# Performance work log

Measured on AMD Instinct MI355X. Metric: run time of the kernel, lower is better.

Reference implementation:

```python
import jax, jax.numpy as jnp
import numpy as np

B, S, K, N, G = 4, 16, 8192, 8192, 128
NUM_GROUPS = K // G

def setup_inputs() -> dict:
    key = jax.random.key(0)
    k1, k2, k3, k4, k5 = jax.random.split(key, 5)
    x = jax.random.normal(k1, (B, S, K), dtype=jnp.float32)
    qweight = jax.random.randint(k2, (K, N), -128, 128, dtype=jnp.int32)
    # small positive scales like real quantizers produce
    scales = jax.random.uniform(k3, (NUM_GROUPS, N), dtype=jnp.float32) * 0.01 + 1e-4
    zeros = jax.random.uniform(k4, (NUM_GROUPS, N), dtype=jnp.float32) * 2.0 - 1.0
    bias = jax.random.normal(k5, (N,), dtype=jnp.float32)
    return {"x": x, "qweight": qweight, "scales": scales, "zeros": zeros,
            "bias": bias, "group_size": G}

def reference(x, qweight, scales, zeros, bias, group_size):
    # Expand per-group scale/zero along K: [num_groups, N] -> [K, N]
    Kdim = qweight.shape[0]
    if scales.shape[0] == 1:
        scale_exp = jnp.broadcast_to(scales, (Kdim, scales.shape[1]))
        zero_exp = jnp.broadcast_to(zeros, (Kdim, zeros.shape[1]))
    else:
        scale_exp = jnp.repeat(scales, group_size, axis=0)[:Kdim]
        zero_exp = jnp.repeat(zeros, group_size, axis=0)[:Kdim]
    # Dequantize: W[k, n] = (q - zero) * scale
    weight_fp = (qweight.astype(x.dtype) - zero_exp) * scale_exp  # [K, N]
    out = jnp.einsum('bsk,kn->bsn', x, weight_fp) + bias
    return out
```

## Files before the change

### kernel.cpp

```cpp
#include <hip/hip_runtime.h>

typedef __attribute__((ext_vector_type(8))) short short8;
typedef __attribute__((ext_vector_type(8))) unsigned short ushort8;
typedef __attribute__((ext_vector_type(4))) unsigned short ushort4v;
typedef __attribute__((ext_vector_type(4))) int int4v;
typedef __attribute__((ext_vector_type(4))) float f32x4;

#define Mdim 64
#define Kdim 8192
#define Ndim 8192
#define GRP 128
#define NGRP 64
#define KSPLIT 4
#define NG2 (NGRP / KSPLIT)
#define BN 128

#define SWZ(row, kk) ((row)*128 + ((kk) ^ (8*((((row) >> 3) ^ (row)) & 7))))

__device__ __forceinline__ unsigned short f2bf(float f) {
    unsigned int u = __builtin_bit_cast(unsigned int, f);
    u += 0x7FFFu + ((u >> 16) & 1u);
    return (unsigned short)(u >> 16);
}
__device__ __forceinline__ float bf2f(unsigned short h) {
    unsigned int u = ((unsigned int)h) << 16;
    return __builtin_bit_cast(float, u);
}

__global__ void prep_kernel(const float* __restrict__ x,
                            unsigned short* __restrict__ xh,
                            unsigned short* __restrict__ xl,
                            float* __restrict__ xsum) {
    const int tid = threadIdx.x;
    const int u = blockIdx.x * 8 + (tid >> 5);
    const int g = u & (NGRP - 1);
    const int m = u >> 6;
    const int lane = tid & 31;
    const int k = g * GRP + lane * 4;
    f32x4 v = *(const f32x4*)(x + (size_t)m * Kdim + k);
    ushort4v hv, lv;
    float s = 0.f;
#pragma unroll
    for (int i = 0; i < 4; ++i) {
        unsigned short h = f2bf(v[i]);
        hv[i] = h;
        lv[i] = f2bf(v[i] - bf2f(h));
        s += v[i];
    }
    *(ushort4v*)(xh + (size_t)m * Kdim + k) = hv;
    *(ushort4v*)(xl + (size_t)m * Kdim + k) = lv;
#pragma unroll
    for (int off = 16; off > 0; off >>= 1) s += __shfl_down(s, off, 32);
    if (lane == 0) xsum[g * Mdim + m] = s;
}

__launch_bounds__(512, 2)
__global__ void qlin_kernel(const unsigned short* __restrict__ xh,
                            const unsigned short* __restrict__ xl,
                            const int* __restrict__ qw,
                            const float* __restrict__ scales,
                            const float* __restrict__ zeros,
                            const float* __restrict__ xsum,
                            float* __restrict__ pout) {
    __shared__ unsigned short lq[2][128 * 128];
    __shared__ unsigned short lxh[2][64 * 128];
    __shared__ unsigned short lxl[2][64 * 128];
    __shared__ float ls[NG2][128];
    __shared__ float lz[NG2][128];
    __shared__ float lxs[NG2][64];

    const int tid = threadIdx.x;
    const int kh = blockIdx.x & (KSPLIT - 1);
    const int n0 = (blockIdx.x >> 2) * BN;
    const int g0 = kh * NG2;

    const int w = tid >> 6;
    const int l = tid & 63;
    const int lcol = l & 15;
    const int lhi = l >> 4;
    const int mt = (w >> 2) * 32;
    const int ns = (w & 3) * 32;

    const int qc = tid & 31;
    const int qr = tid >> 5;
    const int xc = tid & 15;
    const int xm = tid >> 4;

    const int c0 = n0 + ns + lcol;
    const int c1 = c0 + 16;

    int4v qv[8];
    ushort8 xga, xgb, xgc, xgd;

    auto LOADX = [&](int g) {
        const size_t kb = (size_t)g * GRP + xc * 8;
        xga = *(const ushort8*)(xh + (size_t)xm * Kdim + kb);
        xgb = *(const ushort8*)(xh + (size_t)(xm + 32) * Kdim + kb);
        xgc = *(const ushort8*)(xl + (size_t)xm * Kdim + kb);
        xgd = *(const ushort8*)(xl + (size_t)(xm + 32) * Kdim + kb);
    };
    auto LOADQ = [&](int g) {
        const size_t kb = (size_t)g * GRP + qr * 8;
        const int nc = n0 + qc * 4;
#pragma unroll
        for (int j = 0; j < 8; ++j)
            qv[j] = *(const int4v*)(qw + (kb + j) * Ndim + nc);
    };
    auto WRITEX = [&](int b) {
        *(ushort8*)&lxh[b][SWZ(xm, xc * 8)] = xga;
        *(ushort8*)&lxh[b][SWZ(xm + 32, xc * 8)] = xgb;
        *(ushort8*)&lxl[b][SWZ(xm, xc * 8)] = xgc;
        *(ushort8*)&lxl[b][SWZ(xm + 32, xc * 8)] = xgd;
    };
    auto WRITEQ = [&](int b) {
#pragma unroll
        for (int i = 0; i < 4; ++i) {
            int4v pk;
#pragma unroll
            for (int t = 0; t < 4; ++t) {
                unsigned lo = __builtin_bit_cast(unsigned, (float)qv[2 * t][i]) >> 16;
                unsigned hi = __builtin_bit_cast(unsigned, (float)qv[2 * t + 1][i]) & 0xFFFF0000u;
                pk[t] = (int)(lo | hi);
            }
            *(int4v*)&lq[b][SWZ(qc * 4 + i, qr * 8)] = pk;
        }
    };

    f32x4 acc00 = {0,0,0,0}, acc01 = {0,0,0,0}, acc10 = {0,0,0,0}, acc11 = {0,0,0,0};

    {
        const int tg = tid >> 5, tc = tid & 31;
        f32x4 sv = *(const f32x4*)(scales + (size_t)(g0 + tg) * Ndim + n0 + tc * 4);
        f32x4 zv = *(const f32x4*)(zeros + (size_t)(g0 + tg) * Ndim + n0 + tc * 4);
        float x0 = xsum[(g0 + (tid >> 6)) * Mdim + (tid & 63)];
        float x1 = xsum[(g0 + ((tid + 512) >> 6)) * Mdim + (tid & 63)];
        LOADX(g0);
        LOADQ(g0);
        *(f32x4*)&ls[tg][tc * 4] = sv;
        *(f32x4*)&lz[tg][tc * 4] = zv;
        (&lxs[0][0])[tid] = x0;
        (&lxs[0][0])[tid + 512] = x1;
        WRITEX(0);
        WRITEQ(0);
        if (1 < NG2) { LOADX(g0 + 1); LOADQ(g0 + 1); }
        asm volatile("s_waitcnt lgkmcnt(0)" ::: "memory");
        __builtin_amdgcn_s_barrier();
    }

    for (int g = 0; g < NG2; ++g) {
        const int b = g & 1;

        f32x4 p00 = {0,0,0,0}, p01 = {0,0,0,0}, p10 = {0,0,0,0}, p11 = {0,0,0,0};
#pragma unroll
        for (int ks = 0; ks < 4; ++ks) {
            const int kk = ks * 32 + lhi * 8;
            short8 bq0 = *(const short8*)&lq[b][SWZ(ns + lcol, kk)];
            short8 bq1 = *(const short8*)&lq[b][SWZ(ns + 16 + lcol, kk)];
            short8 ah0 = *(const short8*)&lxh[b][SWZ(mt + lcol, kk)];
            short8 al0 = *(const short8*)&lxl[b][SWZ(mt + lcol, kk)];
            short8 ah1 = *(const short8*)&lxh[b][SWZ(mt + 16 + lcol, kk)];
            short8 al1 = *(const short8*)&lxl[b][SWZ(mt + 16 + lcol, kk)];
            p00 = __builtin_amdgcn_mfma_f32_16x16x32_bf16(ah0, bq0, p00, 0, 0, 0);
            p00 = __builtin_amdgcn_mfma_f32_16x16x32_bf16(al0, bq0, p00, 0, 0, 0);
            p01 = __builtin_amdgcn_mfma_f32_16x16x32_bf16(ah0, bq1, p01, 0, 0, 0);
            p01 = __builtin_amdgcn_mfma_f32_16x16x32_bf16(al0, bq1, p01, 0, 0, 0);
            p10 = __builtin_amdgcn_mfma_f32_16x16x32_bf16(ah1, bq0, p10, 0, 0, 0);
            p10 = __builtin_amdgcn_mfma_f32_16x16x32_bf16(al1, bq0, p10, 0, 0, 0);
            p11 = __builtin_amdgcn_mfma_f32_16x16x32_bf16(ah1, bq1, p11, 0, 0, 0);
            p11 = __builtin_amdgcn_mfma_f32_16x16x32_bf16(al1, bq1, p11, 0, 0, 0);
        }
        {
            const float s0 = ls[g][ns + lcol],      z0 = lz[g][ns + lcol];
            const float s1 = ls[g][ns + 16 + lcol], z1 = lz[g][ns + 16 + lcol];
            f32x4 xs0 = *(const f32x4*)&lxs[g][mt + lhi * 4];
            f32x4 xs1 = *(const f32x4*)&lxs[g][mt + 16 + lhi * 4];
#pragma unroll
            for (int r = 0; r < 4; ++r) {
                acc00[r] += s0 * (p00[r] - z0 * xs0[r]);
                acc01[r] += s1 * (p01[r] - z1 * xs0[r]);
                acc10[r] += s0 * (p10[r] - z0 * xs1[r]);
                acc11[r] += s1 * (p11[r] - z1 * xs1[r]);
            }
        }

        if (g + 1 < NG2) {
            WRITEX(b ^ 1);
            if (g + 2 < NG2) {
                LOADX(g0 + g + 2);
                __builtin_amdgcn_sched_barrier(0);
            }
            WRITEQ(b ^ 1);
            if (g + 2 < NG2) {
                LOADQ(g0 + g + 2);
                __builtin_amdgcn_sched_barrier(0);
            }
            asm volatile("s_waitcnt lgkmcnt(0)" ::: "memory");
            __builtin_amdgcn_s_barrier();
        }
    }

    const size_t ob = (size_t)kh * Mdim * Ndim;
#pragma unroll
    for (int r = 0; r < 4; ++r) {
        pout[ob + (size_t)(mt + lhi * 4 + r) * Ndim + c0] = acc00[r];
        pout[ob + (size_t)(mt + lhi * 4 + r) * Ndim + c1] = acc01[r];
        pout[ob + (size_t)(mt + 16 + lhi * 4 + r) * Ndim + c0] = acc10[r];
        pout[ob + (size_t)(mt + 16 + lhi * 4 + r) * Ndim + c1] = acc11[r];
    }
}

__global__ void reduce_kernel(const float* __restrict__ pout,
                              const float* __restrict__ bias,
                              float* __restrict__ out) {
    const size_t e = ((size_t)blockIdx.x * 256 + threadIdx.x) * 4;
    const int n = (int)(e & (Ndim - 1));
    f32x4 a = *(const f32x4*)(bias + n);
#pragma unroll
    for (int s = 0; s < KSPLIT; ++s) {
        f32x4 ppart = *(const f32x4*)(pout + (size_t)s * Mdim * Ndim + e);
#pragma unroll
        for (int r = 0; r < 4; ++r) a[r] += ppart[r];
    }
    *(f32x4*)(out + e) = a;
}

extern "C" void kernel_launch(void* const* d_in, const int* in_sizes, int n_in,
                              void* d_out, int out_size, void* d_ws, size_t ws_size,
                              hipStream_t stream) {
    const float* x = (const float*)d_in[0];
    const int* qw = (const int*)d_in[1];
    const float* scales = (const float*)d_in[2];
    const float* zeros = (const float*)d_in[3];
    const float* bias = (const float*)d_in[4];

    unsigned short* xh = (unsigned short*)d_ws;
    unsigned short* xl = xh + (size_t)Mdim * Kdim;
    float* xsum = (float*)(xl + (size_t)Mdim * Kdim);
    float* pout = xsum + NGRP * Mdim;
    float* out = (float*)d_out;

    prep_kernel<<<512, 256, 0, stream>>>(x, xh, xl, xsum);
    qlin_kernel<<<(Ndim / BN) * KSPLIT, 512, 0, stream>>>(xh, xl, qw, scales, zeros, xsum, pout);
    reduce_kernel<<<(Mdim * Ndim / 4) / 256, 256, 0, stream>>>(pout, bias, out);
}
```

Measured before the change: 56.23 us.

## Deepen weight prefetch to three stages and replace split-K reduction with atomics

Quantized weight tiles are now prefetched two groups ahead using two alternating register sets, so global load latency has more time to hide behind MFMA work. The split-K partial-sum buffer and the separate reduce kernel are removed. Instead, an init kernel writes the bias into the output and each K-split block atomically adds its tile. This cuts the partial-sum write and re-read traffic, but it adds atomic contention, more register pressure from the extra weight buffer, and a non-deterministic summation order.

```diff
diff --git a/kernel.cpp b/kernel.cpp
--- a/kernel.cpp
+++ b/kernel.cpp
@@ -54,6 +54,35 @@
     if (lane == 0) xsum[g * Mdim + m] = s;
 }
 
+__global__ void init_kernel(const float* __restrict__ bias,
+                            float* __restrict__ out) {
+    const size_t e = ((size_t)blockIdx.x * 256 + threadIdx.x) * 4;
+    const int n = (int)(e & (Ndim - 1));
+    *(f32x4*)(out + e) = *(const f32x4*)(bias + n);
+}
+
+#define LOADQ_M(dst, g) do {                                                  \
+    const size_t kb_ = (size_t)(g) * GRP + qr * 8;                            \
+    const int nc_ = n0 + qc * 4;                                              \
+    _Pragma("unroll")                                                         \
+    for (int j = 0; j < 8; ++j)                                               \
+        dst[j] = *(const int4v*)(qw + (kb_ + j) * Ndim + nc_);                \
+} while (0)
+
+#define WRITEQ_M(src, b) do {                                                 \
+    _Pragma("unroll")                                                         \
+    for (int i = 0; i < 4; ++i) {                                             \
+        int4v pk_;                                                            \
+        _Pragma("unroll")                                                     \
+        for (int t = 0; t < 4; ++t) {                                         \
+            unsigned lo_ = __builtin_bit_cast(unsigned, (float)src[2*t][i]) >> 16;           \
+            unsigned hi_ = __builtin_bit_cast(unsigned, (float)src[2*t+1][i]) & 0xFFFF0000u; \
+            pk_[t] = (int)(lo_ | hi_);                                        \
+        }                                                                     \
+        *(int4v*)&lq[b][SWZ(qc * 4 + i, qr * 8)] = pk_;                       \
+    }                                                                         \
+} while (0)
+
 __launch_bounds__(512, 2)
 __global__ void qlin_kernel(const unsigned short* __restrict__ xh,
                             const unsigned short* __restrict__ xl,
@@ -61,7 +90,7 @@
                             const float* __restrict__ scales,
                             const float* __restrict__ zeros,
                             const float* __restrict__ xsum,
-                            float* __restrict__ pout) {
+                            float* __restrict__ out) {
     __shared__ unsigned short lq[2][128 * 128];
     __shared__ unsigned short lxh[2][64 * 128];
     __shared__ unsigned short lxl[2][64 * 128];
@@ -89,7 +118,7 @@
     const int c0 = n0 + ns + lcol;
     const int c1 = c0 + 16;
 
-    int4v qv[8];
+    int4v qva[8], qvb[8];
     ushort8 xga, xgb, xgc, xgd;
 
     auto LOADX = [&](int g) {
@@ -99,57 +128,17 @@
         xgc = *(const ushort8*)(xl + (size_t)xm * Kdim + kb);
         xgd = *(const ushort8*)(xl + (size_t)(xm + 32) * Kdim + kb);
     };
-    auto LOADQ = [&](int g) {
-        const size_t kb = (size_t)g * GRP + qr * 8;
-        const int nc = n0 + qc * 4;
-#pragma unroll
-        for (int j = 0; j < 8; ++j)
-            qv[j] = *(const int4v*)(qw + (kb + j) * Ndim + nc);
-    };
     auto WRITEX = [&](int b) {
         *(ushort8*)&lxh[b][SWZ(xm, xc * 8)] = xga;
         *(ushort8*)&lxh[b][SWZ(xm + 32, xc * 8)] = xgb;
         *(ushort8*)&lxl[b][SWZ(xm, xc * 8)] = xgc;
         *(ushort8*)&lxl[b][SWZ(xm + 32, xc * 8)] = xgd;
     };
-    auto WRITEQ = [&](int b) {
-#pragma unroll
-        for (int i = 0; i < 4; ++i) {
-            int4v pk;
-#pragma unroll
-            for (int t = 0; t < 4; ++t) {
-                unsigned lo = __builtin_bit_cast(unsigned, (float)qv[2 * t][i]) >> 16;
-                unsigned hi = __builtin_bit_cast(unsigned, (float)qv[2 * t + 1][i]) & 0xFFFF0000u;
-                pk[t] = (int)(lo | hi);
-            }
-            *(int4v*)&lq[b][SWZ(qc * 4 + i, qr * 8)] = pk;
-        }
-    };
 
     f32x4 acc00 = {0,0,0,0}, acc01 = {0,0,0,0}, acc10 = {0,0,0,0}, acc11 = {0,0,0,0};
 
-    {
-        const int tg = tid >> 5, tc = tid & 31;
-        f32x4 sv = *(const f32x4*)(scales + (size_t)(g0 + tg) * Ndim + n0 + tc * 4);
-        f32x4 zv = *(const f32x4*)(zeros + (size_t)(g0 + tg) * Ndim + n0 + tc * 4);
-        float x0 = xsum[(g0 + (tid >> 6)) * Mdim + (tid & 63)];
-        float x1 = xsum[(g0 + ((tid + 512) >> 6)) * Mdim + (tid & 63)];
-        LOADX(g0);
-        LOADQ(g0);
-        *(f32x4*)&ls[tg][tc * 4] = sv;
-        *(f32x4*)&lz[tg][tc * 4] = zv;
-        (&lxs[0][0])[tid] = x0;
-        (&lxs[0][0])[tid + 512] = x1;
-        WRITEX(0);
-        WRITEQ(0);
-        if (1 < NG2) { LOADX(g0 + 1); LOADQ(g0 + 1); }
-        asm volatile("s_waitcnt lgkmcnt(0)" ::: "memory");
-        __builtin_amdgcn_s_barrier();
-    }
-
-    for (int g = 0; g < NG2; ++g) {
+    auto COMPUTE = [&](int g) {
         const int b = g & 1;
-
         f32x4 p00 = {0,0,0,0}, p01 = {0,0,0,0}, p10 = {0,0,0,0}, p11 = {0,0,0,0};
 #pragma unroll
         for (int ks = 0; ks < 4; ++ks) {
@@ -169,59 +158,72 @@
             p11 = __builtin_amdgcn_mfma_f32_16x16x32_bf16(ah1, bq1, p11, 0, 0, 0);
             p11 = __builtin_amdgcn_mfma_f32_16x16x32_bf16(al1, bq1, p11, 0, 0, 0);
         }
-        {
-            const float s0 = ls[g][ns + lcol],      z0 = lz[g][ns + lcol];
-            const float s1 = ls[g][ns + 16 + lcol], z1 = lz[g][ns + 16 + lcol];
-            f32x4 xs0 = *(const f32x4*)&lxs[g][mt + lhi * 4];
-            f32x4 xs1 = *(const f32x4*)&lxs[g][mt + 16 + lhi * 4];
-#pragma unroll
-            for (int r = 0; r < 4; ++r) {
-                acc00[r] += s0 * (p00[r] - z0 * xs0[r]);
-                acc01[r] += s1 * (p01[r] - z1 * xs0[r]);
-                acc10[r] += s0 * (p10[r] - z0 * xs1[r]);
-                acc11[r] += s1 * (p11[r] - z1 * xs1[r]);
-            }
+        const float s0 = ls[g][ns + lcol],      z0 = lz[g][ns + lcol];
+        const float s1 = ls[g][ns + 16 + lcol], z1 = lz[g][ns + 16 + lcol];
+        f32x4 xs0 = *(const f32x4*)&lxs[g][mt + lhi * 4];
+        f32x4 xs1 = *(const f32x4*)&lxs[g][mt + 16 + lhi * 4];
+#pragma unroll
+        for (int r = 0; r < 4; ++r) {
+            acc00[r] += s0 * (p00[r] - z0 * xs0[r]);
+            acc01[r] += s1 * (p01[r] - z1 * xs0[r]);
+            acc10[r] += s0 * (p10[r] - z0 * xs1[r]);
+            acc11[r] += s1 * (p11[r] - z1 * xs1[r]);
         }
-
-        if (g + 1 < NG2) {
-            WRITEX(b ^ 1);
-            if (g + 2 < NG2) {
-                LOADX(g0 + g + 2);
-                __builtin_amdgcn_sched_barrier(0);
-            }
-            WRITEQ(b ^ 1);
-            if (g + 2 < NG2) {
-                LOADQ(g0 + g + 2);
-                __builtin_amdgcn_sched_barrier(0);
-            }
-            asm volatile("s_waitcnt lgkmcnt(0)" ::: "memory");
-            __builtin_amdgcn_s_barrier();
-        }
-    }
-
-    const size_t ob = (size_t)kh * Mdim * Ndim;
+    };
+
+    {
+        const int tg = tid >> 5, tc = tid & 31;
+        f32x4 sv = *(const f32x4*)(scales + (size_t)(g0 + tg) * Ndim + n0 + tc * 4);
+        f32x4 zv = *(const f32x4*)(zeros + (size_t)(g0 + tg) * Ndim + n0 + tc * 4);
+        float x0 = xsum[(g0 + (tid >> 6)) * Mdim + (tid & 63)];
+        float x1 = xsum[(g0 + ((tid + 512) >> 6)) * Mdim + (tid & 63)];
+        LOADX(g0);
+        LOADQ_M(qva, g0);
+        *(f32x4*)&ls[tg][tc * 4] = sv;
+        *(f32x4*)&lz[tg][tc * 4] = zv;
+        (&lxs[0][0])[tid] = x0;
+        (&lxs[0][0])[tid + 512] = x1;
+        WRITEX(0);
+        WRITEQ_M(qva, 0);
+        LOADX(g0 + 1);
+        LOADQ_M(qvb, g0 + 1);
+        LOADQ_M(qva, g0 + 2);
+        asm volatile("s_waitcnt lgkmcnt(0)" ::: "memory");
+        __builtin_amdgcn_s_barrier();
+    }
+
+#define STEP(G, DSET) do {                                                    \
+    const int g_ = (G);                                                       \
+    COMPUTE(g_);                                                              \
+    if (g_ + 1 < NG2) {                                                       \
+        WRITEX((g_ & 1) ^ 1);                      \
+        if (g_ + 2 < NG2) {                                                   \
+            LOADX(g0 + g_ + 2);                                               \
+            __builtin_amdgcn_sched_barrier(0);                                \
+        }                                                                     \
+        WRITEQ_M(DSET, (g_ & 1) ^ 1);              \
+        if (g_ + 3 < NG2) {                                                   \
+            LOADQ_M(DSET, g0 + g_ + 3);             \
+            __builtin_amdgcn_sched_barrier(0);                                \
+        }                                                                     \
+        asm volatile("s_waitcnt lgkmcnt(0)" ::: "memory");                    \
+        __builtin_amdgcn_s_barrier();                                         \
+    }                                                                         \
+} while (0)
+
+    for (int gg = 0; gg < NG2; gg += 2) {
+        STEP(gg, qvb);
+        STEP(gg + 1, qva);
+    }
+#undef STEP
+
 #pragma unroll
     for (int r = 0; r < 4; ++r) {
-        pout[ob + (size_t)(mt + lhi * 4 + r) * Ndim + c0] = acc00[r];
-        pout[ob + (size_t)(mt + lhi * 4 + r) * Ndim + c1] = acc01[r];
-        pout[ob + (size_t)(mt + 16 + lhi * 4 + r) * Ndim + c0] = acc10[r];
-        pout[ob + (size_t)(mt + 16 + lhi * 4 + r) * Ndim + c1] = acc11[r];
-    }
-}
-
-__global__ void reduce_kernel(const float* __restrict__ pout,
-                              const float* __restrict__ bias,
-                              float* __restrict__ out) {
-    const size_t e = ((size_t)blockIdx.x * 256 + threadIdx.x) * 4;
-    const int n = (int)(e & (Ndim - 1));
-    f32x4 a = *(const f32x4*)(bias + n);
-#pragma unroll
-    for (int s = 0; s < KSPLIT; ++s) {
-        f32x4 ppart = *(const f32x4*)(pout + (size_t)s * Mdim * Ndim + e);
-#pragma unroll
-        for (int r = 0; r < 4; ++r) a[r] += ppart[r];
-    }
-    *(f32x4*)(out + e) = a;
+        atomicAdd(out + (size_t)(mt + lhi * 4 + r) * Ndim + c0, acc00[r]);
+        atomicAdd(out + (size_t)(mt + lhi * 4 + r) * Ndim + c1, acc01[r]);
+        atomicAdd(out + (size_t)(mt + 16 + lhi * 4 + r) * Ndim + c0, acc10[r]);
+        atomicAdd(out + (size_t)(mt + 16 + lhi * 4 + r) * Ndim + c1, acc11[r]);
+    }
 }
 
 extern "C" void kernel_launch(void* const* d_in, const int* in_sizes, int n_in,
@@ -236,10 +238,9 @@
     unsigned short* xh = (unsigned short*)d_ws;
     unsigned short* xl = xh + (size_t)Mdim * Kdim;
     float* xsum = (float*)(xl + (size_t)Mdim * Kdim);
-    float* pout = xsum + NGRP * Mdim;
     float* out = (float*)d_out;
 
     prep_kernel<<<512, 256, 0, stream>>>(x, xh, xl, xsum);
-    qlin_kernel<<<(Ndim / BN) * KSPLIT, 512, 0, stream>>>(xh, xl, qw, scales, zeros, xsum, pout);
-    reduce_kernel<<<(Mdim * Ndim / 4) / 256, 256, 0, stream>>>(pout, bias, out);
-}
+    init_kernel<<<(Mdim * Ndim / 4) / 256, 256, 0, stream>>>(bias, out);
+    qlin_kernel<<<(Ndim / BN) * KSPLIT, 512, 0, stream>>>(xh, xl, qw, scales, zeros, xsum, out);
+}
```

After: 58.27 us. +3.6%, slower.

## Fuse split-K reduction into GEMM kernel via last-block atomic counter

Applied to the files above, without the earlier changes.

Removes the separate reduce kernel launch. Each N-tile keeps an atomic counter, reset in the prep kernel, and the last split-K block to finish sums the partial outputs plus bias for its tile. This saves one kernel launch and lets the reduction overlap with other blocks still computing. The cost is a threadfence, an atomic per block, and serial reduce work in the final block of each tile.

```diff
diff --git a/kernel.cpp b/kernel.cpp
--- a/kernel.cpp
+++ b/kernel.cpp
@@ -30,8 +30,10 @@
 __global__ void prep_kernel(const float* __restrict__ x,
                             unsigned short* __restrict__ xh,
                             unsigned short* __restrict__ xl,
-                            float* __restrict__ xsum) {
+                            float* __restrict__ xsum,
+                            int* __restrict__ cnt) {
     const int tid = threadIdx.x;
+    if (blockIdx.x == 0 && tid < 64) cnt[tid] = 0;
     const int u = blockIdx.x * 8 + (tid >> 5);
     const int g = u & (NGRP - 1);
     const int m = u >> 6;
@@ -61,17 +63,22 @@
                             const float* __restrict__ scales,
                             const float* __restrict__ zeros,
                             const float* __restrict__ xsum,
-                            float* __restrict__ pout) {
+                            float* __restrict__ pout,
+                            int* __restrict__ cnt,
+                            const float* __restrict__ bias,
+                            float* __restrict__ out) {
     __shared__ unsigned short lq[2][128 * 128];
     __shared__ unsigned short lxh[2][64 * 128];
     __shared__ unsigned short lxl[2][64 * 128];
     __shared__ float ls[NG2][128];
     __shared__ float lz[NG2][128];
     __shared__ float lxs[NG2][64];
+    __shared__ int lflag;
 
     const int tid = threadIdx.x;
     const int kh = blockIdx.x & (KSPLIT - 1);
-    const int n0 = (blockIdx.x >> 2) * BN;
+    const int nt = blockIdx.x >> 2;
+    const int n0 = nt * BN;
     const int g0 = kh * NG2;
 
     const int w = tid >> 6;
@@ -142,7 +149,8 @@
         (&lxs[0][0])[tid + 512] = x1;
         WRITEX(0);
         WRITEQ(0);
-        if (1 < NG2) { LOADX(g0 + 1); LOADQ(g0 + 1); }
+        LOADX(g0 + 1);
+        LOADQ(g0 + 1);
         asm volatile("s_waitcnt lgkmcnt(0)" ::: "memory");
         __builtin_amdgcn_s_barrier();
     }
@@ -207,21 +215,29 @@
         pout[ob + (size_t)(mt + 16 + lhi * 4 + r) * Ndim + c0] = acc10[r];
         pout[ob + (size_t)(mt + 16 + lhi * 4 + r) * Ndim + c1] = acc11[r];
     }
-}
-
-__global__ void reduce_kernel(const float* __restrict__ pout,
-                              const float* __restrict__ bias,
-                              float* __restrict__ out) {
-    const size_t e = ((size_t)blockIdx.x * 256 + threadIdx.x) * 4;
-    const int n = (int)(e & (Ndim - 1));
-    f32x4 a = *(const f32x4*)(bias + n);
-#pragma unroll
-    for (int s = 0; s < KSPLIT; ++s) {
-        f32x4 ppart = *(const f32x4*)(pout + (size_t)s * Mdim * Ndim + e);
-#pragma unroll
-        for (int r = 0; r < 4; ++r) a[r] += ppart[r];
-    }
-    *(f32x4*)(out + e) = a;
+
+    __threadfence();
+    __syncthreads();
+    if (tid == 0) lflag = atomicAdd(&cnt[nt], 1);
+    __syncthreads();
+    if (lflag == KSPLIT - 1) {
+        __threadfence();
+#pragma unroll
+        for (int j = 0; j < 4; ++j) {
+            const int i = tid * 4 + j;
+            const int m = i >> 5;
+            const int c4 = (i & 31) * 4;
+            const size_t e = (size_t)m * Ndim + n0 + c4;
+            f32x4 a = *(const f32x4*)(bias + n0 + c4);
+#pragma unroll
+            for (int s = 0; s < KSPLIT; ++s) {
+                f32x4 pp = *(const f32x4*)(pout + (size_t)s * Mdim * Ndim + e);
+#pragma unroll
+                for (int r = 0; r < 4; ++r) a[r] += pp[r];
+            }
+            *(f32x4*)(out + e) = a;
+        }
+    }
 }
 
 extern "C" void kernel_launch(void* const* d_in, const int* in_sizes, int n_in,
@@ -237,9 +253,10 @@
     unsigned short* xl = xh + (size_t)Mdim * Kdim;
     float* xsum = (float*)(xl + (size_t)Mdim * Kdim);
     float* pout = xsum + NGRP * Mdim;
+    int* cnt = (int*)(pout + (size_t)KSPLIT * Mdim * Ndim);
     float* out = (float*)d_out;
 
-    prep_kernel<<<512, 256, 0, stream>>>(x, xh, xl, xsum);
-    qlin_kernel<<<(Ndim / BN) * KSPLIT, 512, 0, stream>>>(xh, xl, qw, scales, zeros, xsum, pout);
-    reduce_kernel<<<(Mdim * Ndim / 4) / 256, 256, 0, stream>>>(pout, bias, out);
-}
+    prep_kernel<<<512, 256, 0, stream>>>(x, xh, xl, xsum, cnt);
+    qlin_kernel<<<(Ndim / BN) * KSPLIT, 512, 0, stream>>>(xh, xl, qw, scales, zeros,
+                                                          xsum, pout, cnt, bias, out);
+}
```

Result: slower. 140.1 us (+149.1%).

## Fuse x bf16 split into GEMM kernel and compute group sums via MFMA

Applied to the files above, without the earlier changes.

Removes the separate prep kernel. The main kernel now loads fp32 x directly and does the hi/lo bf16 split inside the shared-memory write. Per-group row sums of x, needed for the zero-point correction, are computed with extra MFMAs against a vector of ones instead of being precomputed. This saves one kernel launch and the global round trip for xh/xl/xsum. In exchange, x is converted redundantly in every N-tile block, the global x loads double in size (fp32 instead of bf16), and MFMA work per step grows by half. The ones-based sum uses the bf16 hi+lo split rather than the exact fp32 sum.

```diff
diff --git a/kernel.cpp b/kernel.cpp
--- a/kernel.cpp
+++ b/kernel.cpp
@@ -2,7 +2,6 @@
 
 typedef __attribute__((ext_vector_type(8))) short short8;
 typedef __attribute__((ext_vector_type(8))) unsigned short ushort8;
-typedef __attribute__((ext_vector_type(4))) unsigned short ushort4v;
 typedef __attribute__((ext_vector_type(4))) int int4v;
 typedef __attribute__((ext_vector_type(4))) float f32x4;
 
@@ -27,47 +26,17 @@
     return __builtin_bit_cast(float, u);
 }
 
-__global__ void prep_kernel(const float* __restrict__ x,
-                            unsigned short* __restrict__ xh,
-                            unsigned short* __restrict__ xl,
-                            float* __restrict__ xsum) {
-    const int tid = threadIdx.x;
-    const int u = blockIdx.x * 8 + (tid >> 5);
-    const int g = u & (NGRP - 1);
-    const int m = u >> 6;
-    const int lane = tid & 31;
-    const int k = g * GRP + lane * 4;
-    f32x4 v = *(const f32x4*)(x + (size_t)m * Kdim + k);
-    ushort4v hv, lv;
-    float s = 0.f;
-#pragma unroll
-    for (int i = 0; i < 4; ++i) {
-        unsigned short h = f2bf(v[i]);
-        hv[i] = h;
-        lv[i] = f2bf(v[i] - bf2f(h));
-        s += v[i];
-    }
-    *(ushort4v*)(xh + (size_t)m * Kdim + k) = hv;
-    *(ushort4v*)(xl + (size_t)m * Kdim + k) = lv;
-#pragma unroll
-    for (int off = 16; off > 0; off >>= 1) s += __shfl_down(s, off, 32);
-    if (lane == 0) xsum[g * Mdim + m] = s;
-}
-
 __launch_bounds__(512, 2)
-__global__ void qlin_kernel(const unsigned short* __restrict__ xh,
-                            const unsigned short* __restrict__ xl,
+__global__ void qlin_kernel(const float* __restrict__ x,
                             const int* __restrict__ qw,
                             const float* __restrict__ scales,
                             const float* __restrict__ zeros,
-                            const float* __restrict__ xsum,
                             float* __restrict__ pout) {
     __shared__ unsigned short lq[2][128 * 128];
     __shared__ unsigned short lxh[2][64 * 128];
     __shared__ unsigned short lxl[2][64 * 128];
     __shared__ float ls[NG2][128];
     __shared__ float lz[NG2][128];
-    __shared__ float lxs[NG2][64];
 
     const int tid = threadIdx.x;
     const int kh = blockIdx.x & (KSPLIT - 1);
@@ -90,14 +59,18 @@
     const int c1 = c0 + 16;
 
     int4v qv[8];
-    ushort8 xga, xgb, xgc, xgd;
+    f32x4 xva, xvb, xvc, xvd;
+
+    short8 ones;
+#pragma unroll
+    for (int i = 0; i < 8; ++i) ones[i] = (short)0x3F80;
 
     auto LOADX = [&](int g) {
         const size_t kb = (size_t)g * GRP + xc * 8;
-        xga = *(const ushort8*)(xh + (size_t)xm * Kdim + kb);
-        xgb = *(const ushort8*)(xh + (size_t)(xm + 32) * Kdim + kb);
-        xgc = *(const ushort8*)(xl + (size_t)xm * Kdim + kb);
-        xgd = *(const ushort8*)(xl + (size_t)(xm + 32) * Kdim + kb);
+        xva = *(const f32x4*)(x + (size_t)xm * Kdim + kb);
+        xvb = *(const f32x4*)(x + (size_t)xm * Kdim + kb + 4);
+        xvc = *(const f32x4*)(x + (size_t)(xm + 32) * Kdim + kb);
+        xvd = *(const f32x4*)(x + (size_t)(xm + 32) * Kdim + kb + 4);
     };
     auto LOADQ = [&](int g) {
         const size_t kb = (size_t)g * GRP + qr * 8;
@@ -107,10 +80,19 @@
             qv[j] = *(const int4v*)(qw + (kb + j) * Ndim + nc);
     };
     auto WRITEX = [&](int b) {
-        *(ushort8*)&lxh[b][SWZ(xm, xc * 8)] = xga;
-        *(ushort8*)&lxh[b][SWZ(xm + 32, xc * 8)] = xgb;
-        *(ushort8*)&lxl[b][SWZ(xm, xc * 8)] = xgc;
-        *(ushort8*)&lxl[b][SWZ(xm + 32, xc * 8)] = xgd;
+        ushort8 h0, l0, h1, l1;
+#pragma unroll
+        for (int i = 0; i < 4; ++i) {
+            unsigned short h;
+            h = f2bf(xva[i]); h0[i] = h;     l0[i] = f2bf(xva[i] - bf2f(h));
+            h = f2bf(xvb[i]); h0[4 + i] = h; l0[4 + i] = f2bf(xvb[i] - bf2f(h));
+            h = f2bf(xvc[i]); h1[i] = h;     l1[i] = f2bf(xvc[i] - bf2f(h));
+            h = f2bf(xvd[i]); h1[4 + i] = h; l1[4 + i] = f2bf(xvd[i] - bf2f(h));
+        }
+        *(ushort8*)&lxh[b][SWZ(xm, xc * 8)] = h0;
+        *(ushort8*)&lxl[b][SWZ(xm, xc * 8)] = l0;
+        *(ushort8*)&lxh[b][SWZ(xm + 32, xc * 8)] = h1;
+        *(ushort8*)&lxl[b][SWZ(xm + 32, xc * 8)] = l1;
     };
     auto WRITEQ = [&](int b) {
 #pragma unroll
@@ -132,17 +114,14 @@
         const int tg = tid >> 5, tc = tid & 31;
         f32x4 sv = *(const f32x4*)(scales + (size_t)(g0 + tg) * Ndim + n0 + tc * 4);
         f32x4 zv = *(const f32x4*)(zeros + (size_t)(g0 + tg) * Ndim + n0 + tc * 4);
-        float x0 = xsum[(g0 + (tid >> 6)) * Mdim + (tid & 63)];
-        float x1 = xsum[(g0 + ((tid + 512) >> 6)) * Mdim + (tid & 63)];
         LOADX(g0);
         LOADQ(g0);
         *(f32x4*)&ls[tg][tc * 4] = sv;
         *(f32x4*)&lz[tg][tc * 4] = zv;
-        (&lxs[0][0])[tid] = x0;
-        (&lxs[0][0])[tid + 512] = x1;
         WRITEX(0);
         WRITEQ(0);
-        if (1 < NG2) { LOADX(g0 + 1); LOADQ(g0 + 1); }
+        LOADX(g0 + 1);
+        LOADQ(g0 + 1);
         asm volatile("s_waitcnt lgkmcnt(0)" ::: "memory");
         __builtin_amdgcn_s_barrier();
     }
@@ -151,6 +130,7 @@
         const int b = g & 1;
 
         f32x4 p00 = {0,0,0,0}, p01 = {0,0,0,0}, p10 = {0,0,0,0}, p11 = {0,0,0,0};
+        f32x4 ps0 = {0,0,0,0}, ps1 = {0,0,0,0};
 #pragma unroll
         for (int ks = 0; ks < 4; ++ks) {
             const int kk = ks * 32 + lhi * 8;
@@ -168,18 +148,20 @@
             p10 = __builtin_amdgcn_mfma_f32_16x16x32_bf16(al1, bq0, p10, 0, 0, 0);
             p11 = __builtin_amdgcn_mfma_f32_16x16x32_bf16(ah1, bq1, p11, 0, 0, 0);
             p11 = __builtin_amdgcn_mfma_f32_16x16x32_bf16(al1, bq1, p11, 0, 0, 0);
+            ps0 = __builtin_amdgcn_mfma_f32_16x16x32_bf16(ah0, ones, ps0, 0, 0, 0);
+            ps0 = __builtin_amdgcn_mfma_f32_16x16x32_bf16(al0, ones, ps0, 0, 0, 0);
+            ps1 = __builtin_amdgcn_mfma_f32_16x16x32_bf16(ah1, ones, ps1, 0, 0, 0);
+            ps1 = __builtin_amdgcn_mfma_f32_16x16x32_bf16(al1, ones, ps1, 0, 0, 0);
         }
         {
             const float s0 = ls[g][ns + lcol],      z0 = lz[g][ns + lcol];
             const float s1 = ls[g][ns + 16 + lcol], z1 = lz[g][ns + 16 + lcol];
-            f32x4 xs0 = *(const f32x4*)&lxs[g][mt + lhi * 4];
-            f32x4 xs1 = *(const f32x4*)&lxs[g][mt + 16 + lhi * 4];
 #pragma unroll
             for (int r = 0; r < 4; ++r) {
-                acc00[r] += s0 * (p00[r] - z0 * xs0[r]);
-                acc01[r] += s1 * (p01[r] - z1 * xs0[r]);
-                acc10[r] += s0 * (p10[r] - z0 * xs1[r]);
-                acc11[r] += s1 * (p11[r] - z1 * xs1[r]);
+                acc00[r] += s0 * (p00[r] - z0 * ps0[r]);
+                acc01[r] += s1 * (p01[r] - z1 * ps0[r]);
+                acc10[r] += s0 * (p10[r] - z0 * ps1[r]);
+                acc11[r] += s1 * (p11[r] - z1 * ps1[r]);
             }
         }
 
@@ -233,13 +215,9 @@
     const float* zeros = (const float*)d_in[3];
     const float* bias = (const float*)d_in[4];
 
-    unsigned short* xh = (unsigned short*)d_ws;
-    unsigned short* xl = xh + (size_t)Mdim * Kdim;
-    float* xsum = (float*)(xl + (size_t)Mdim * Kdim);
-    float* pout = xsum + NGRP * Mdim;
+    float* pout = (float*)d_ws;
     float* out = (float*)d_out;
 
-    prep_kernel<<<512, 256, 0, stream>>>(x, xh, xl, xsum);
-    qlin_kernel<<<(Ndim / BN) * KSPLIT, 512, 0, stream>>>(xh, xl, qw, scales, zeros, xsum, pout);
+    qlin_kernel<<<(Ndim / BN) * KSPLIT, 512, 0, stream>>>(x, qw, scales, zeros, pout);
     reduce_kernel<<<(Mdim * Ndim / 4) / 256, 256, 0, stream>>>(pout, bias, out);
 }
```

Result: no change. 56.15 us (-0.1%).
